# Kernel tuning notes

Hardware: AMD Instinct MI355X
Metric: run time of the kernel (lower is better)

Reference implementation:

```python
import jax, jax.numpy as jnp
import numpy as np

N_NODES = 50000
N_EDGES = 800000
D_IN, D_HID, D_OUT = 64, 128, 64


def _graph_conv(x, src, dst, w_rel, w_root, b):
    # PyG GraphConv with aggr='sum':
    #   out_i = W_rel @ sum_{j in N(i)} x_j + W_root @ x_i + b
    # Aggregate first at input width (sum commutes with the linear map),
    # then apply the two linear transforms.
    agg = jax.ops.segment_sum(x[src], dst, num_segments=x.shape[0])  # [N, d_in]
    return agg @ w_rel + x @ w_root + b


def setup_inputs() -> dict:
    key = jax.random.key(0)
    ks = jax.random.split(key, 9)
    x = jax.random.normal(ks[0], (N_NODES, D_IN), dtype=jnp.float32)
    edge_index = jax.random.randint(ks[1], (2, N_EDGES), 0, N_NODES, dtype=jnp.int64)

    def glorot(k, fan_in, fan_out):
        s = jnp.sqrt(2.0 / (fan_in + fan_out)).astype(jnp.float32)
        return jax.random.normal(k, (fan_in, fan_out), dtype=jnp.float32) * s

    return {
        "x": x,
        "edge_index": edge_index,
        "w_rel1": glorot(ks[2], D_IN, D_HID),  "w_root1": glorot(ks[3], D_IN, D_HID),  "b1": jnp.zeros((D_HID,), jnp.float32),
        "w_rel2": glorot(ks[4], D_HID, D_HID), "w_root2": glorot(ks[5], D_HID, D_HID), "b2": jnp.zeros((D_HID,), jnp.float32),
        "w_rel3": glorot(ks[6], D_HID, D_OUT), "w_root3": glorot(ks[7], D_HID, D_OUT), "b3": jnp.zeros((D_OUT,), jnp.float32),
    }


def reference(x, edge_index, w_rel1, w_root1, b1, w_rel2, w_root2, b2, w_rel3, w_root3, b3):
    src, dst = edge_index[0], edge_index[1]
    h = jax.nn.relu(_graph_conv(x, src, dst, w_rel1, w_root1, b1))
    h = jax.nn.relu(_graph_conv(h, src, dst, w_rel2, w_root2, b2))
    out = _graph_conv(h, src, dst, w_rel3, w_root3, b3)  # final layer: no relu
    return out
```

## Files before the change

kernel.cpp:

```cpp
#include <hip/hip_runtime.h>
#include <hip/hip_bf16.h>


#define N_D_IN 64
#define N_D_HID 128
#define N_D_OUT 64

__global__ void detect_kernel(const unsigned int* __restrict__ w, int* __restrict__ flag) {
    __shared__ int nonzero;
    if (threadIdx.x == 0) nonzero = 0;
    __syncthreads();
    for (int i = threadIdx.x; i < 1024; i += 256) {
        if (w[2 * i + 1] != 0u) atomicOr(&nonzero, 1);
    }
    __syncthreads();
    if (threadIdx.x == 0) *flag = (nonzero ? 0 : 1);
}

__device__ __forceinline__ int load_edge(const void* edge, const int* flag, size_t idx) {
    if (*flag) return (int)((const long long*)edge)[idx];
    return ((const int*)edge)[idx];
}

__global__ void hist_kernel(const void* __restrict__ edge, const int* __restrict__ flag,
                            int* __restrict__ cnt, int n_edges) {
    int i = blockIdx.x * 256 + threadIdx.x;
    if (i >= n_edges) return;
    int d = load_edge(edge, flag, (size_t)n_edges + i);
    atomicAdd(&cnt[d], 1);
}

__global__ __launch_bounds__(1024) void scan_kernel(const int* __restrict__ cnt,
                                                    int* __restrict__ row_ptr,
                                                    int* __restrict__ cursor, int n) {
    __shared__ int part[1024];
    int t = threadIdx.x;
    int C = (n + 1023) / 1024;
    int lo = t * C, hi = min(lo + C, n);
    int s = 0;
    for (int i = lo; i < hi; ++i) s += cnt[i];
    part[t] = s;
    __syncthreads();
    for (int off = 1; off < 1024; off <<= 1) {
        int v = (t >= off) ? part[t - off] : 0;
        __syncthreads();
        part[t] += v;
        __syncthreads();
    }
    int run = (t == 0) ? 0 : part[t - 1];
    for (int i = lo; i < hi; ++i) {
        int c = cnt[i];
        row_ptr[i] = run;
        cursor[i] = run;
        run += c;
    }
    if (t == 1023) row_ptr[n] = run;
}

__global__ void scatter_kernel(const void* __restrict__ edge, const int* __restrict__ flag,
                               int* __restrict__ cursor, int* __restrict__ srcs, int n_edges) {
    int i = blockIdx.x * 256 + threadIdx.x;
    if (i >= n_edges) return;
    int s = load_edge(edge, flag, (size_t)i);
    int d = load_edge(edge, flag, (size_t)n_edges + i);
    int pos = atomicAdd(&cursor[d], 1);
    srcs[pos] = s;
}

template <int D, bool ADD_BASE>
__global__ __launch_bounds__(64) void agg_kernel(const float* __restrict__ in,
                                                 const float* __restrict__ base,
                                                 float* __restrict__ out,
                                                 const int* __restrict__ row_ptr,
                                                 const int* __restrict__ srcs, int n_nodes) {
    constexpr int LPR = D / 4;
    constexpr int SLOTS = 64 / LPR;
    const int node = blockIdx.x;
    const int lane = threadIdx.x;
    const int c4 = lane % LPR;
    const int slot = lane / LPR;
    const int e0 = row_ptr[node], e1 = row_ptr[node + 1];
    float4 acc = make_float4(0.f, 0.f, 0.f, 0.f);
    for (int e = e0 + slot; e < e1; e += SLOTS) {
        int s = srcs[e];
        float4 v = *(const float4*)&in[(size_t)s * D + c4 * 4];
        acc.x += v.x; acc.y += v.y; acc.z += v.z; acc.w += v.w;
    }
#pragma unroll
    for (int off = LPR; off < 64; off <<= 1) {
        acc.x += __shfl_xor(acc.x, off);
        acc.y += __shfl_xor(acc.y, off);
        acc.z += __shfl_xor(acc.z, off);
        acc.w += __shfl_xor(acc.w, off);
    }
    if (lane < LPR) {
        if (ADD_BASE) {
            float4 b = *(const float4*)&base[(size_t)node * D + c4 * 4];
            acc.x += b.x; acc.y += b.y; acc.z += b.z; acc.w += b.w;
        }
        *(float4*)&out[(size_t)node * D + c4 * 4] = acc;
    }
}

template <int DIN, int DOUT, bool DUAL, bool RELU, bool BIAS>
__global__ __launch_bounds__(256) void gemm_kernel(const float* __restrict__ A,
                                                   const float* __restrict__ B,
                                                   const float* __restrict__ W1,
                                                   const float* __restrict__ W2,
                                                   const float* __restrict__ bias,
                                                   float* __restrict__ out, int n_nodes) {
    constexpr int BN = 32;
    constexpr int TJ = 4;
    constexpr int JS = DOUT / TJ;
    constexpr int NL = 256 / JS;
    constexpr int TM = BN / NL;
    constexpr int K4 = DIN / 4;
    constexpr int PAD = 4;

    __shared__ float lA[BN][DIN + PAD];
    __shared__ float lB[DUAL ? BN : 1][DUAL ? (DIN + PAD) : 4];

    const int tid = threadIdx.x;
    const int node0 = blockIdx.x * BN;

    for (int idx = tid; idx < BN * K4; idx += 256) {
        int n = idx / K4, k4 = idx % K4;
        int gn = node0 + n;
        float4 av = make_float4(0.f, 0.f, 0.f, 0.f);
        float4 bv = make_float4(0.f, 0.f, 0.f, 0.f);
        if (gn < n_nodes) {
            av = *(const float4*)&A[(size_t)gn * DIN + k4 * 4];
            if constexpr (DUAL) bv = *(const float4*)&B[(size_t)gn * DIN + k4 * 4];
        }
        *(float4*)&lA[n][k4 * 4] = av;
        if constexpr (DUAL) *(float4*)&lB[n][k4 * 4] = bv;
    }
    __syncthreads();

    const int js = tid % JS;
    const int j0 = js * TJ;
    const int nbase = (tid / JS) * TM;

    float acc[TM][TJ];
#pragma unroll
    for (int m = 0; m < TM; ++m)
#pragma unroll
        for (int c = 0; c < TJ; ++c) acc[m][c] = 0.f;

    for (int k4 = 0; k4 < K4; ++k4) {
        float w1s[4][4], w2s[4][4];
#pragma unroll
        for (int u = 0; u < 4; ++u) {
            int k = k4 * 4 + u;
            float4 t = *(const float4*)&W1[(size_t)k * DOUT + j0];
            w1s[u][0] = t.x; w1s[u][1] = t.y; w1s[u][2] = t.z; w1s[u][3] = t.w;
            if constexpr (DUAL) {
                float4 t2 = *(const float4*)&W2[(size_t)k * DOUT + j0];
                w2s[u][0] = t2.x; w2s[u][1] = t2.y; w2s[u][2] = t2.z; w2s[u][3] = t2.w;
            }
        }
#pragma unroll
        for (int m = 0; m < TM; ++m) {
            float4 a4 = *(const float4*)&lA[nbase + m][k4 * 4];
            float a[4] = {a4.x, a4.y, a4.z, a4.w};
#pragma unroll
            for (int c = 0; c < TJ; ++c)
#pragma unroll
                for (int u = 0; u < 4; ++u) acc[m][c] += a[u] * w1s[u][c];
            if constexpr (DUAL) {
                float4 b4 = *(const float4*)&lB[nbase + m][k4 * 4];
                float b[4] = {b4.x, b4.y, b4.z, b4.w};
#pragma unroll
                for (int c = 0; c < TJ; ++c)
#pragma unroll
                    for (int u = 0; u < 4; ++u) acc[m][c] += b[u] * w2s[u][c];
            }
        }
    }

    float bv[TJ] = {0.f, 0.f, 0.f, 0.f};
    if constexpr (BIAS) {
        float4 t = *(const float4*)&bias[j0];
        bv[0] = t.x; bv[1] = t.y; bv[2] = t.z; bv[3] = t.w;
    }
#pragma unroll
    for (int m = 0; m < TM; ++m) {
        int gn = node0 + nbase + m;
        if (gn < n_nodes) {
            float4 o;
            float v0 = acc[m][0] + bv[0], v1 = acc[m][1] + bv[1];
            float v2 = acc[m][2] + bv[2], v3 = acc[m][3] + bv[3];
            if constexpr (RELU) {
                v0 = fmaxf(v0, 0.f); v1 = fmaxf(v1, 0.f);
                v2 = fmaxf(v2, 0.f); v3 = fmaxf(v3, 0.f);
            }
            o.x = v0; o.y = v1; o.z = v2; o.w = v3;
            *(float4*)&out[(size_t)gn * DOUT + j0] = o;
        }
    }
}

extern "C" void kernel_launch(void* const* d_in, const int* in_sizes, int n_in,
                              void* d_out, int out_size, void* d_ws, size_t ws_size,
                              hipStream_t stream) {
    const float* x = (const float*)d_in[0];
    const void* edge = d_in[1];
    const float* w_rel1 = (const float*)d_in[2];
    const float* w_root1 = (const float*)d_in[3];
    const float* b1 = (const float*)d_in[4];
    const float* w_rel2 = (const float*)d_in[5];
    const float* w_root2 = (const float*)d_in[6];
    const float* b2 = (const float*)d_in[7];
    const float* w_rel3 = (const float*)d_in[8];
    const float* w_root3 = (const float*)d_in[9];
    const float* b3 = (const float*)d_in[10];
    float* out = (float*)d_out;

    const int n_nodes = in_sizes[0] / N_D_IN;
    const int n_edges = in_sizes[1] / 2;

    char* ws = (char*)d_ws;
    int* cnt = (int*)(ws + 0);
    int* row_ptr = (int*)(ws + (1 << 20));
    int* cursor = (int*)(ws + (2 << 20));
    int* flag = (int*)(ws + (3 << 20));
    int* srcs = (int*)(ws + (3 << 20) + 256);
    float* agg = (float*)(ws + (size_t)(7 << 20));
    float* h1 = (float*)(ws + (size_t)(32 << 20));
    float* h2 = (float*)(ws + (size_t)(57 << 20));
    float* t3 = (float*)(ws + (size_t)(32 << 20));
    float* base3 = (float*)(ws + (size_t)(45 << 20));

    const int eblk = (n_edges + 255) / 256;
    const int gblk = (n_nodes + 31) / 32;

    hipMemsetAsync(cnt, 0, (size_t)n_nodes * sizeof(int), stream);
    detect_kernel<<<1, 256, 0, stream>>>((const unsigned int*)edge, flag);
    hist_kernel<<<eblk, 256, 0, stream>>>(edge, flag, cnt, n_edges);
    scan_kernel<<<1, 1024, 0, stream>>>(cnt, row_ptr, cursor, n_nodes);
    scatter_kernel<<<eblk, 256, 0, stream>>>(edge, flag, cursor, srcs, n_edges);

    agg_kernel<64, false><<<n_nodes, 64, 0, stream>>>(x, nullptr, agg, row_ptr, srcs, n_nodes);
    gemm_kernel<64, 128, true, true, true><<<gblk, 256, 0, stream>>>(
        agg, x, w_rel1, w_root1, b1, h1, n_nodes);

    agg_kernel<128, false><<<n_nodes, 64, 0, stream>>>(h1, nullptr, agg, row_ptr, srcs, n_nodes);
    gemm_kernel<128, 128, true, true, true><<<gblk, 256, 0, stream>>>(
        agg, h1, w_rel2, w_root2, b2, h2, n_nodes);

    gemm_kernel<128, 64, false, false, false><<<gblk, 256, 0, stream>>>(
        h2, nullptr, w_rel3, nullptr, nullptr, t3, n_nodes);
    gemm_kernel<128, 64, false, false, true><<<gblk, 256, 0, stream>>>(
        h2, nullptr, w_root3, nullptr, b3, base3, n_nodes);
    agg_kernel<64, true><<<n_nodes, 64, 0, stream>>>(t3, base3, out, row_ptr, srcs, n_nodes);
}
```

Before: 549.0 us.

## Parallelize CSR scan, pack four nodes per agg block, fuse layer-3 GEMMs

Replaces the single-block serial prefix scan with a three-kernel multi-block scan: block sums, a scan of those sums, then per-block emit. The aggregation kernel now handles four nodes per 256-thread block instead of one node per 64-thread block, which cuts block count and scheduling overhead. The two layer-3 GEMMs that both read h2 are fused into a single kernel that writes both outputs, so h2 is loaded once. This adds kernel launches to the scan path and raises register pressure in the fused GEMM.

```diff
diff --git a/kernel.cpp b/kernel.cpp
--- a/kernel.cpp
+++ b/kernel.cpp
@@ -30,31 +30,56 @@
     atomicAdd(&cnt[d], 1);
 }
 
-__global__ __launch_bounds__(1024) void scan_kernel(const int* __restrict__ cnt,
-                                                    int* __restrict__ row_ptr,
-                                                    int* __restrict__ cursor, int n) {
-    __shared__ int part[1024];
+__global__ __launch_bounds__(256) void blocksum_kernel(const int* __restrict__ cnt,
+                                                       int* __restrict__ bsum, int n) {
+    int i = blockIdx.x * 256 + threadIdx.x;
+    int v = (i < n) ? cnt[i] : 0;
+#pragma unroll
+    for (int off = 1; off < 64; off <<= 1) v += __shfl_xor(v, off);
+    __shared__ int wsums[4];
+    if ((threadIdx.x & 63) == 0) wsums[threadIdx.x >> 6] = v;
+    __syncthreads();
+    if (threadIdx.x == 0) bsum[blockIdx.x] = wsums[0] + wsums[1] + wsums[2] + wsums[3];
+}
+
+__global__ __launch_bounds__(1024) void scan_bsum_kernel(const int* __restrict__ bsum,
+                                                         int* __restrict__ boff, int nb) {
+    __shared__ int tmp[1024];
     int t = threadIdx.x;
-    int C = (n + 1023) / 1024;
-    int lo = t * C, hi = min(lo + C, n);
-    int s = 0;
-    for (int i = lo; i < hi; ++i) s += cnt[i];
-    part[t] = s;
+    int v = (t < nb) ? bsum[t] : 0;
+    tmp[t] = v;
     __syncthreads();
     for (int off = 1; off < 1024; off <<= 1) {
-        int v = (t >= off) ? part[t - off] : 0;
+        int u = (t >= off) ? tmp[t - off] : 0;
         __syncthreads();
-        part[t] += v;
+        tmp[t] += u;
         __syncthreads();
     }
-    int run = (t == 0) ? 0 : part[t - 1];
-    for (int i = lo; i < hi; ++i) {
-        int c = cnt[i];
-        row_ptr[i] = run;
-        cursor[i] = run;
-        run += c;
-    }
-    if (t == 1023) row_ptr[n] = run;
+    if (t < nb) boff[t] = tmp[t] - v;
+}
+
+__global__ __launch_bounds__(256) void emit_kernel(const int* __restrict__ cnt,
+                                                   const int* __restrict__ boff,
+                                                   int* __restrict__ row_ptr,
+                                                   int* __restrict__ cursor, int n) {
+    __shared__ int tmp[256];
+    int b = blockIdx.x, t = threadIdx.x;
+    int i = b * 256 + t;
+    int v = (i < n) ? cnt[i] : 0;
+    tmp[t] = v;
+    __syncthreads();
+    for (int off = 1; off < 256; off <<= 1) {
+        int u = (t >= off) ? tmp[t - off] : 0;
+        __syncthreads();
+        tmp[t] += u;
+        __syncthreads();
+    }
+    int excl = tmp[t] - v + boff[b];
+    if (i < n) {
+        row_ptr[i] = excl;
+        cursor[i] = excl;
+        if (i == n - 1) row_ptr[n] = excl + v;
+    }
 }
 
 __global__ void scatter_kernel(const void* __restrict__ edge, const int* __restrict__ flag,
@@ -68,15 +93,16 @@
 }
 
 template <int D, bool ADD_BASE>
-__global__ __launch_bounds__(64) void agg_kernel(const float* __restrict__ in,
-                                                 const float* __restrict__ base,
-                                                 float* __restrict__ out,
-                                                 const int* __restrict__ row_ptr,
-                                                 const int* __restrict__ srcs, int n_nodes) {
+__global__ __launch_bounds__(256) void agg_kernel(const float* __restrict__ in,
+                                                  const float* __restrict__ base,
+                                                  float* __restrict__ out,
+                                                  const int* __restrict__ row_ptr,
+                                                  const int* __restrict__ srcs, int n_nodes) {
     constexpr int LPR = D / 4;
     constexpr int SLOTS = 64 / LPR;
-    const int node = blockIdx.x;
-    const int lane = threadIdx.x;
+    const int node = blockIdx.x * 4 + (threadIdx.x >> 6);
+    if (node >= n_nodes) return;
+    const int lane = threadIdx.x & 63;
     const int c4 = lane % LPR;
     const int slot = lane / LPR;
     const int e0 = row_ptr[node], e1 = row_ptr[node + 1];
@@ -196,6 +222,86 @@
             }
             o.x = v0; o.y = v1; o.z = v2; o.w = v3;
             *(float4*)&out[(size_t)gn * DOUT + j0] = o;
+        }
+    }
+}
+
+template <int DIN, int DOUT>
+__global__ __launch_bounds__(256) void gemm2out_kernel(const float* __restrict__ A,
+                                                       const float* __restrict__ W1,
+                                                       const float* __restrict__ W2,
+                                                       const float* __restrict__ bias,
+                                                       float* __restrict__ o1,
+                                                       float* __restrict__ o2, int n_nodes) {
+    constexpr int BN = 32;
+    constexpr int TJ = 4;
+    constexpr int JS = DOUT / TJ;
+    constexpr int NL = 256 / JS;
+    constexpr int TM = BN / NL;
+    constexpr int K4 = DIN / 4;
+    constexpr int PAD = 4;
+
+    __shared__ float lA[BN][DIN + PAD];
+
+    const int tid = threadIdx.x;
+    const int node0 = blockIdx.x * BN;
+
+    for (int idx = tid; idx < BN * K4; idx += 256) {
+        int n = idx / K4, k4 = idx % K4;
+        int gn = node0 + n;
+        float4 av = make_float4(0.f, 0.f, 0.f, 0.f);
+        if (gn < n_nodes) av = *(const float4*)&A[(size_t)gn * DIN + k4 * 4];
+        *(float4*)&lA[n][k4 * 4] = av;
+    }
+    __syncthreads();
+
+    const int js = tid % JS;
+    const int j0 = js * TJ;
+    const int nbase = (tid / JS) * TM;
+
+    float acc1[TM][TJ], acc2[TM][TJ];
+#pragma unroll
+    for (int m = 0; m < TM; ++m)
+#pragma unroll
+        for (int c = 0; c < TJ; ++c) { acc1[m][c] = 0.f; acc2[m][c] = 0.f; }
+
+    for (int k4 = 0; k4 < K4; ++k4) {
+        float w1s[4][4], w2s[4][4];
+#pragma unroll
+        for (int u = 0; u < 4; ++u) {
+            int k = k4 * 4 + u;
+            float4 t = *(const float4*)&W1[(size_t)k * DOUT + j0];
+            w1s[u][0] = t.x; w1s[u][1] = t.y; w1s[u][2] = t.z; w1s[u][3] = t.w;
+            float4 t2 = *(const float4*)&W2[(size_t)k * DOUT + j0];
+            w2s[u][0] = t2.x; w2s[u][1] = t2.y; w2s[u][2] = t2.z; w2s[u][3] = t2.w;
+        }
+#pragma unroll
+        for (int m = 0; m < TM; ++m) {
+            float4 a4 = *(const float4*)&lA[nbase + m][k4 * 4];
+            float a[4] = {a4.x, a4.y, a4.z, a4.w};
+#pragma unroll
+            for (int c = 0; c < TJ; ++c)
+#pragma unroll
+                for (int u = 0; u < 4; ++u) {
+                    acc1[m][c] += a[u] * w1s[u][c];
+                    acc2[m][c] += a[u] * w2s[u][c];
+                }
+        }
+    }
+
+    float4 bt = *(const float4*)&bias[j0];
+    float bv[4] = {bt.x, bt.y, bt.z, bt.w};
+#pragma unroll
+    for (int m = 0; m < TM; ++m) {
+        int gn = node0 + nbase + m;
+        if (gn < n_nodes) {
+            float4 q;
+            q.x = acc1[m][0]; q.y = acc1[m][1]; q.z = acc1[m][2]; q.w = acc1[m][3];
+            *(float4*)&o1[(size_t)gn * DOUT + j0] = q;
+            float4 r;
+            r.x = acc2[m][0] + bv[0]; r.y = acc2[m][1] + bv[1];
+            r.z = acc2[m][2] + bv[2]; r.w = acc2[m][3] + bv[3];
+            *(float4*)&o2[(size_t)gn * DOUT + j0] = r;
         }
     }
 }
@@ -224,33 +330,37 @@
     int* row_ptr = (int*)(ws + (1 << 20));
     int* cursor = (int*)(ws + (2 << 20));
     int* flag = (int*)(ws + (3 << 20));
-    int* srcs = (int*)(ws + (3 << 20) + 256);
-    float* agg = (float*)(ws + (size_t)(7 << 20));
-    float* h1 = (float*)(ws + (size_t)(32 << 20));
-    float* h2 = (float*)(ws + (size_t)(57 << 20));
-    float* t3 = (float*)(ws + (size_t)(32 << 20));
-    float* base3 = (float*)(ws + (size_t)(45 << 20));
+    int* bsum = (int*)(ws + (3 << 20) + 1024);
+    int* boff = (int*)(ws + (3 << 20) + 1024 + 4096);
+    int* srcs = (int*)(ws + (4 << 20));
+    float* agg = (float*)(ws + (size_t)(8 << 20));
+    float* h1 = (float*)(ws + (size_t)(34 << 20));
+    float* h2 = (float*)(ws + (size_t)(60 << 20));
+    float* t3 = (float*)(ws + (size_t)(34 << 20));
+    float* base3 = (float*)(ws + (size_t)(47 << 20));
 
     const int eblk = (n_edges + 255) / 256;
+    const int nblk = (n_nodes + 255) / 256;
     const int gblk = (n_nodes + 31) / 32;
+    const int ablk = (n_nodes + 3) / 4;
 
     hipMemsetAsync(cnt, 0, (size_t)n_nodes * sizeof(int), stream);
     detect_kernel<<<1, 256, 0, stream>>>((const unsigned int*)edge, flag);
     hist_kernel<<<eblk, 256, 0, stream>>>(edge, flag, cnt, n_edges);
-    scan_kernel<<<1, 1024, 0, stream>>>(cnt, row_ptr, cursor, n_nodes);
+    blocksum_kernel<<<nblk, 256, 0, stream>>>(cnt, bsum, n_nodes);
+    scan_bsum_kernel<<<1, 1024, 0, stream>>>(bsum, boff, nblk);
+    emit_kernel<<<nblk, 256, 0, stream>>>(cnt, boff, row_ptr, cursor, n_nodes);
     scatter_kernel<<<eblk, 256, 0, stream>>>(edge, flag, cursor, srcs, n_edges);
 
-    agg_kernel<64, false><<<n_nodes, 64, 0, stream>>>(x, nullptr, agg, row_ptr, srcs, n_nodes);
+    agg_kernel<64, false><<<ablk, 256, 0, stream>>>(x, nullptr, agg, row_ptr, srcs, n_nodes);
     gemm_kernel<64, 128, true, true, true><<<gblk, 256, 0, stream>>>(
         agg, x, w_rel1, w_root1, b1, h1, n_nodes);
 
-    agg_kernel<128, false><<<n_nodes, 64, 0, stream>>>(h1, nullptr, agg, row_ptr, srcs, n_nodes);
+    agg_kernel<128, false><<<ablk, 256, 0, stream>>>(h1, nullptr, agg, row_ptr, srcs, n_nodes);
     gemm_kernel<128, 128, true, true, true><<<gblk, 256, 0, stream>>>(
         agg, h1, w_rel2, w_root2, b2, h2, n_nodes);
 
-    gemm_kernel<128, 64, false, false, false><<<gblk, 256, 0, stream>>>(
-        h2, nullptr, w_rel3, nullptr, nullptr, t3, n_nodes);
-    gemm_kernel<128, 64, false, false, true><<<gblk, 256, 0, stream>>>(
-        h2, nullptr, w_root3, nullptr, b3, base3, n_nodes);
-    agg_kernel<64, true><<<n_nodes, 64, 0, stream>>>(t3, base3, out, row_ptr, srcs, n_nodes);
-}
+    gemm2out_kernel<128, 64><<<gblk, 256, 0, stream>>>(
+        h2, w_rel3, w_root3, b3, t3, base3, n_nodes);
+    agg_kernel<64, true><<<ablk, 256, 0, stream>>>(t3, base3, out, row_ptr, srcs, n_nodes);
+}
```

Measured after the change: 451.9 us. 17.7% less time.
